# Performance work log

Measured on AMD Instinct MI355X. Metric: run time of the kernel, lower is better.

The kernel has to match this reference:

```python
import jax, jax.numpy as jnp
import numpy as np

B, M = 2, 8192          # clouds per batch, points per cloud (N = B*M)
K_NEAR, K_FAR, K_SMOOTH = 8, 16, 8
T_LOC, T_CON = 0.1, 0.5
EPS = 1e-8


def setup_inputs() -> dict:
    key = jax.random.key(0)
    k1, k2 = jax.random.split(key)
    scores = jax.random.uniform(k1, (B * M,), dtype=jnp.float32)          # in [0,1]
    coords = jax.random.normal(k2, (B * M, 3), dtype=jnp.float32) * 2.0   # point positions
    batch_ids = (jnp.arange(B * M, dtype=jnp.int32) // M).astype(jnp.int32)
    return {"scores": scores, "coords": coords, "batch_ids": batch_ids}


def _knn_global(coords):
    """Per-cloud brute-force kNN (self included as first neighbor, like pointops.knn_query).
    coords: (N,3) -> global indices (N, K_FAR)."""
    c = coords.reshape(B, M, 3)

    def per_cloud(cb):  # cb: (M,3)
        sq = jnp.sum(cb * cb, axis=-1)                      # (M,)
        d2 = sq[:, None] + sq[None, :] - 2.0 * (cb @ cb.T)  # (M,M) squared dists
        _, idx = jax.lax.top_k(-d2, K_FAR)                  # (M,K_FAR) smallest dists
        return idx

    idx = jax.vmap(per_cloud)(c)                            # (B,M,K_FAR) local indices
    idx = idx + (jnp.arange(B, dtype=idx.dtype) * M)[:, None, None]
    return idx.reshape(B * M, K_FAR)


def _loss_terms(scores, coords, idx):
    # --- locality: neighbors (incl. self) should have similar scores ---
    nb = idx[:, :K_NEAR]                                    # (N,k)
    score_diff = jnp.abs(scores[:, None] - scores[nb])      # (N,k)
    dists = jnp.linalg.norm(coords[:, None, :] - coords[nb], axis=2)  # (N,k)
    w = jnp.exp(-dists / T_LOC)
    loss_loc = jnp.sum(w * score_diff ** 2) / jnp.clip(jnp.sum(w), 1e-8)

    # --- contrastive: near similar, far dissimilar ---
    sim_pos = 1.0 - jnp.abs(scores[:, None] - scores[idx[:, :K_NEAR]])
    sim_neg = 1.0 - jnp.abs(scores[:, None] - scores[idx[:, K_NEAR:K_FAR]])
    loss_pos = -jnp.mean(jnp.log(jax.nn.sigmoid(sim_pos / T_CON) + EPS))
    loss_neg = -jnp.mean(jnp.log(1.0 - jax.nn.sigmoid(sim_neg / T_CON) + EPS))
    loss_con = loss_pos + loss_neg

    # --- distribution: sorted scores match uniform linspace per cloud ---
    sb = jnp.sort(scores.reshape(B, M), axis=1)             # (B,M)
    target = jnp.linspace(0.0, 1.0, M, dtype=scores.dtype)  # (M,)
    loss_dist = jnp.mean(jnp.mean((sb - target[None, :]) ** 2, axis=1))

    # --- smoothness: score close to neighbor mean ---
    nmean = jnp.mean(scores[idx[:, :K_SMOOTH]], axis=1)     # (N,)
    loss_smooth = jnp.mean((scores - nmean) ** 2)

    return loss_loc, loss_con, loss_dist, loss_smooth


def reference(scores, coords, batch_ids):
    del batch_ids  # equal-sized clouds; batch structure is (B, M) by construction
    idx = _knn_global(coords)
    l_loc, l_con, l_dist, l_smooth = _loss_terms(scores, coords, idx)
    total = 1.0 * l_loc + 0.5 * l_con + 0.3 * l_dist + 0.2 * l_smooth
    return total
```

## Files before the change

### kernel.cpp

```cpp
#include <hip/hip_runtime.h>
#include <math.h>

#define BB 2
#define MM 8192
#define NN (BB * MM)
#define NBATCH (NN / 16)
#define NCELL 4096
#define LOSS_BLOCKS 1024

#define PART_OFF   0
#define RANK_OFF   24576
#define IDX_OFF    90112
#define PK_OFF     1138688
#define SS_OFF     1400832
#define DONE_OFF   1466368
#define BBLO_OFF   1597440
#define BBHI_OFF   1613824

__device__ __forceinline__ unsigned mort3(unsigned x, unsigned y, unsigned z) {
    unsigned m = 0;
#pragma unroll
    for (int i = 0; i < 4; ++i) {
        m |= ((x >> i) & 1u) << (3 * i);
        m |= ((y >> i) & 1u) << (3 * i + 1);
        m |= ((z >> i) & 1u) << (3 * i + 2);
    }
    return m;
}

__global__ __launch_bounds__(1024) void prep_kernel(
    const float* __restrict__ coords, const float* __restrict__ scores,
    float4* __restrict__ pk_s, float* __restrict__ s_s,
    float4* __restrict__ bb_lo, float4* __restrict__ bb_hi,
    unsigned* __restrict__ done) {
    __shared__ int hist[NCELL];
    __shared__ int wsum[16];
    const int tid = threadIdx.x, blk = blockIdx.x;
    const int pbase = blk * MM;
    for (int i = tid; i < NCELL; i += 1024) hist[i] = 0;
    if (blk == 0 && tid == 0) *done = 0u;
    __syncthreads();

    int   cid[8];
    float px[8], py[8], pz[8];
#pragma unroll
    for (int it = 0; it < 8; ++it) {
        const int i = pbase + it * 1024 + tid;
        float x = coords[3 * i], y = coords[3 * i + 1], z = coords[3 * i + 2];
        int cx = min(15, max(0, (int)floorf(x) + 8));
        int cy = min(15, max(0, (int)floorf(y) + 8));
        int cz = min(15, max(0, (int)floorf(z) + 8));
        cid[it] = (int)mort3((unsigned)cx, (unsigned)cy, (unsigned)cz);
        px[it] = x; py[it] = y; pz[it] = z;
        atomicAdd(&hist[cid[it]], 1);
    }
    __syncthreads();

    int v[4]; int run = 0;
#pragma unroll
    for (int i = 0; i < 4; ++i) { int t = hist[tid * 4 + i]; v[i] = run; run += t; }
    const int lane = tid & 63, wv = tid >> 6;
    int inc = run;
#pragma unroll
    for (int off = 1; off < 64; off <<= 1) {
        int y = __shfl_up(inc, off);
        if (lane >= off) inc += y;
    }
    int laneExcl = inc - run;
    if (lane == 63) wsum[wv] = inc;
    __syncthreads();
    int wbase = 0;
#pragma unroll
    for (int w = 0; w < 16; ++w) wbase += (w < wv) ? wsum[w] : 0;
    const int base = wbase + laneExcl;
#pragma unroll
    for (int i = 0; i < 4; ++i) hist[tid * 4 + i] = base + v[i];
    __syncthreads();

#pragma unroll
    for (int it = 0; it < 8; ++it) {
        const int pos = pbase + atomicAdd(&hist[cid[it]], 1);
        const float x = px[it], y = py[it], z = pz[it];
        const float sq = fmaf(x, x, fmaf(y, y, z * z));
        pk_s[pos] = make_float4(x, y, z, sq);
        s_s[pos] = scores[pbase + it * 1024 + tid];
    }
    __syncthreads();

    if (tid < 512) {
        const int b = blk * 512 + tid;
        float4 c = pk_s[b * 16];
        float lx = c.x, ly = c.y, lz = c.z, hx = c.x, hy = c.y, hz = c.z;
#pragma unroll
        for (int i = 1; i < 16; ++i) {
            c = pk_s[b * 16 + i];
            lx = fminf(lx, c.x); ly = fminf(ly, c.y); lz = fminf(lz, c.z);
            hx = fmaxf(hx, c.x); hy = fmaxf(hy, c.y); hz = fmaxf(hz, c.z);
        }
        bb_lo[b] = make_float4(lx, ly, lz, 0.f);
        bb_hi[b] = make_float4(hx, hy, hz, 0.f);
    }
}

__device__ __forceinline__ void sort16(unsigned (&a)[16]) {
#pragma unroll
    for (int p2 = 1; p2 < 16; p2 <<= 1) {
#pragma unroll
        for (int k2 = p2; k2 >= 1; k2 >>= 1) {
#pragma unroll
            for (int j2 = k2 % p2; j2 + k2 < 16; j2 += 2 * k2) {
#pragma unroll
                for (int i2 = 0; i2 < k2; ++i2) {
                    if (i2 + j2 + k2 < 16) {
                        if (((i2 + j2) / (2 * p2)) == ((i2 + j2 + k2) / (2 * p2))) {
                            unsigned x = a[i2 + j2], y = a[i2 + j2 + k2];
                            a[i2 + j2]      = min(x, y);
                            a[i2 + j2 + k2] = max(x, y);
                        }
                    }
                }
            }
        }
    }
}

__device__ __forceinline__ void truncmerge(unsigned (&slot)[16], const unsigned (&kb)[16]) {
    unsigned m[16];
#pragma unroll
    for (int k = 0; k < 16; ++k) m[k] = min(slot[k], kb[15 - k]);
#pragma unroll
    for (int st = 8; st >= 1; st >>= 1) {
#pragma unroll
        for (int i = 0; i < 16; ++i) {
            if ((i & st) == 0) {
                unsigned lo = min(m[i], m[i + st]);
                unsigned hi = max(m[i], m[i + st]);
                m[i] = lo; m[i + st] = hi;
            }
        }
    }
#pragma unroll
    for (int k = 0; k < 16; ++k) slot[k] = m[k];
}

__global__ __launch_bounds__(1024) void knnrank_kernel(const float4* __restrict__ pk_s,
                                                       const float* __restrict__ s_s,
                                                       const float4* __restrict__ bb_lo,
                                                       const float4* __restrict__ bb_hi,
                                                       int* __restrict__ out_idx,
                                                       int* __restrict__ out_rank) {
    __shared__ unsigned lds_k[16][16][64];
    __shared__ int lds_aux[16][64];
    __shared__ unsigned lds_tmin[64];
    const int tid = threadIdx.x, lane = tid & 63;
    const int wv = __builtin_amdgcn_readfirstlane(tid >> 6);

    if (blockIdx.x >= 256) {
        const int qbase = (blockIdx.x - 256) << 6;
        const int cloudbase = (qbase >> 13) << 13;
        const float s = s_s[qbase + lane];
        const float* __restrict__ sc = s_s + cloudbase;
        int rk = 0;
        const int j0 = wv * 512;
        for (int jj = 0; jj < 512; jj += 16) {
#pragma unroll
            for (int i = 0; i < 16; ++i) {
                rk += (sc[j0 + jj + i] < s) ? 1 : 0;
            }
        }
        lds_aux[wv][lane] = rk;
        __syncthreads();
        if (wv == 0) {
            int rsum = 0;
#pragma unroll
            for (int w = 0; w < 16; ++w) rsum += lds_aux[w][lane];
            out_rank[qbase + lane] = rsum;
        }
        return;
    }

    const int qbase = blockIdx.x * 64;
    const int cloudbase = (qbase >> 13) << 13;
    const float4 p = pk_s[qbase + lane];
    const int sb0 = (qbase - cloudbase) >> 4;
    const float4* __restrict__ pc = pk_s + cloudbase;
    const int bbase = cloudbase >> 4;

    if (tid < 64) lds_tmin[tid] = 0x7f7fffffu;

    unsigned slot[16];
#pragma unroll
    for (int k = 0; k < 16; ++k) slot[k] = 0x7F000000u + (unsigned)k;
    float t_f = 3.0e38f;

    auto batch = [&](int bi) {
        unsigned kb[16];
#pragma unroll
        for (int i = 0; i < 16; ++i) {
            const int j = bi * 16 + i;
            const float4 c = pc[j];
            float dot = fmaf(p.x, c.x, fmaf(p.y, c.y, p.z * c.z));
            float d2  = fmaf(-2.0f, dot, p.w + c.w);
            kb[i] = (__float_as_uint(d2) & 0xFFFFE000u) | (unsigned)j;
        }
        sort16(kb);
        truncmerge(slot, kb);
        const unsigned nt = (slot[15] & 0xFFFFE000u) + 0x2000u;
        const float ntf = __uint_as_float(nt);
        if (ntf < t_f) {
            t_f = ntf;
            atomicMin(&lds_tmin[lane], nt);
        }
    };

    const int r = sb0 & 15;
    const int ownb = (wv >= r && wv < r + 4) ? (sb0 + (wv - r)) : -1;
    __syncthreads();
    if (ownb >= 0) batch(ownb);
    lds_aux[wv][lane] = (int)__float_as_uint(t_f);
    __syncthreads();
    float tb = __uint_as_float((unsigned)lds_aux[0][lane]);
#pragma unroll
    for (int w = 1; w < 16; ++w) tb = fminf(tb, __uint_as_float((unsigned)lds_aux[w][lane]));
    t_f = fminf(t_f, tb);

    float4 lo = bb_lo[bbase + wv];
    float4 hi = bb_hi[bbase + wv];
    for (int k = 0; k < 32; ++k) {
        const int bi = wv + (k << 4);
        float4 lo_n, hi_n;
        if (k + 1 < 32) {
            lo_n = bb_lo[bbase + bi + 16];
            hi_n = bb_hi[bbase + bi + 16];
        }
        if (bi != ownb) {
            const unsigned tmb = *((volatile unsigned*)&lds_tmin[lane]);
            const float tsh = fminf(t_f, __uint_as_float(tmb));
            float dx = fmaxf(fmaxf(lo.x - p.x, p.x - hi.x), 0.f);
            float dy = fmaxf(fmaxf(lo.y - p.y, p.y - hi.y), 0.f);
            float dz = fmaxf(fmaxf(lo.z - p.z, p.z - hi.z), 0.f);
            float lb = fmaf(dx, dx, fmaf(dy, dy, dz * dz));
            if (__any(fmaf(lb, 0.999f, -1e-5f) < tsh)) batch(bi);
        }
        lo = lo_n; hi = hi_n;
    }

#pragma unroll
    for (int k = 0; k < 16; ++k) lds_k[wv][k][lane] = slot[k];

    for (int half = 8; half >= 1; half >>= 1) {
        __syncthreads();
        if (wv < half) {
            unsigned a[16], m[16];
#pragma unroll
            for (int k = 0; k < 16; ++k) a[k] = lds_k[wv][k][lane];
#pragma unroll
            for (int k = 0; k < 16; ++k) m[k] = min(a[k], lds_k[wv + half][15 - k][lane]);
#pragma unroll
            for (int st = 8; st >= 1; st >>= 1) {
#pragma unroll
                for (int i = 0; i < 16; ++i) {
                    if ((i & st) == 0) {
                        unsigned lo2 = min(m[i], m[i + st]);
                        unsigned hi2 = max(m[i], m[i + st]);
                        m[i] = lo2; m[i + st] = hi2;
                    }
                }
            }
#pragma unroll
            for (int k = 0; k < 16; ++k) lds_k[wv][k][lane] = m[k];
        }
    }
    __syncthreads();

    if (wv == 0) {
#pragma unroll
        for (int k = 0; k < 16; ++k)
            out_idx[(qbase + lane) * 16 + k] = (int)(lds_k[0][k][lane] & 0x1FFFu) + cloudbase;
    }
}

__global__ __launch_bounds__(256) void lossfin_kernel(const float* __restrict__ s_s,
                                                      const float4* __restrict__ pk_s,
                                                      const int* __restrict__ knn,
                                                      const int* __restrict__ rnk,
                                                      float* __restrict__ partial,
                                                      unsigned* __restrict__ done,
                                                      float* __restrict__ out) {
    __shared__ float red[4][6];
    __shared__ float sgrp[16][6];
    __shared__ unsigned lastflag;
    const int t = blockIdx.x * 256 + threadIdx.x;
    const int q = t >> 4, k = t & 15;
    const int nb = knn[t];
    const float s  = s_s[q];
    const float sn = s_s[nb];
    const float diff = fabsf(s - sn);
    const float sim = 1.0f - diff;
    const float sg = 1.0f / (1.0f + expf(-2.0f * sim));

    float a_wd = 0.f, a_w = 0.f, a_pos = 0.f, a_neg = 0.f, snk = 0.f;
    if (k < 8) {
        float4 pq = pk_s[q];
        float4 pn = pk_s[nb];
        float dx = pq.x - pn.x, dy = pq.y - pn.y, dz = pq.z - pn.z;
        float d = sqrtf(dx * dx + dy * dy + dz * dz);
        float w = expf(-10.0f * d);
        a_wd = w * diff * diff;
        a_w  = w;
        a_pos = logf(sg + 1e-8f);
        snk = sn;
    } else {
        a_neg = logf(1.0f - sg + 1e-8f);
    }

    float nsum = snk;
#pragma unroll
    for (int off = 1; off < 16; off <<= 1) nsum += __shfl_xor(nsum, off);

    float a_sm = 0.f, a_di = 0.f;
    if (k == 0) {
        float t1 = s - nsum * 0.125f;
        a_sm = t1 * t1;
        float t2 = s - (float)rnk[q] * (1.0f / 8191.0f);
        a_di = t2 * t2;
    }

#pragma unroll
    for (int off = 1; off < 64; off <<= 1) {
        a_wd  += __shfl_xor(a_wd, off);
        a_w   += __shfl_xor(a_w, off);
        a_pos += __shfl_xor(a_pos, off);
        a_neg += __shfl_xor(a_neg, off);
        a_sm  += __shfl_xor(a_sm, off);
        a_di  += __shfl_xor(a_di, off);
    }
    const int wv = threadIdx.x >> 6;
    if ((threadIdx.x & 63) == 0) {
        red[wv][0] = a_wd; red[wv][1] = a_w; red[wv][2] = a_pos;
        red[wv][3] = a_neg; red[wv][4] = a_sm; red[wv][5] = a_di;
    }
    __syncthreads();
    if (threadIdx.x < 6) {
        float v = red[0][threadIdx.x] + red[1][threadIdx.x] +
                  red[2][threadIdx.x] + red[3][threadIdx.x];
        __hip_atomic_store(&partial[threadIdx.x * LOSS_BLOCKS + blockIdx.x], v,
                           __ATOMIC_RELEASE, __HIP_MEMORY_SCOPE_AGENT);
    }
    __syncthreads();
    if (threadIdx.x == 0)
        lastflag = __hip_atomic_fetch_add(done, 1u, __ATOMIC_ACQ_REL, __HIP_MEMORY_SCOPE_AGENT);
    __syncthreads();

    if (lastflag == (unsigned)(LOSS_BLOCKS - 1)) {
        const int tid = threadIdx.x, lane2 = tid & 63, w4 = tid >> 6;
#pragma unroll
        for (int rep = 0; rep < 4; ++rep) {
            const int w = w4 * 4 + rep;
            float a[6];
#pragma unroll
            for (int term = 0; term < 6; ++term)
                a[term] = __hip_atomic_load(&partial[term * LOSS_BLOCKS + w * 64 + lane2],
                                            __ATOMIC_ACQUIRE, __HIP_MEMORY_SCOPE_AGENT);
#pragma unroll
            for (int off = 1; off < 64; off <<= 1) {
#pragma unroll
                for (int term = 0; term < 6; ++term) a[term] += __shfl_xor(a[term], off);
            }
            if (lane2 == 0) {
#pragma unroll
                for (int term = 0; term < 6; ++term) sgrp[w][term] = a[term];
            }
        }
        __syncthreads();
        if (tid == 0) {
            float acc[6];
#pragma unroll
            for (int term = 0; term < 6; ++term) {
                float v = 0.f;
#pragma unroll
                for (int w = 0; w < 16; ++w) v += sgrp[w][term];
                acc[term] = v;
            }
            float l_loc = acc[0] / fmaxf(acc[1], 1e-8f);
            float l_pos = -acc[2] / (float)(NN * 8);
            float l_neg = -acc[3] / (float)(NN * 8);
            float l_sm  = acc[4] / (float)NN;
            float l_di  = acc[5] / (float)NN;
            out[0] = l_loc + 0.5f * (l_pos + l_neg) + 0.3f * l_di + 0.2f * l_sm;
        }
    }
}

extern "C" void kernel_launch(void* const* d_in, const int* in_sizes, int n_in,
                              void* d_out, int out_size, void* d_ws, size_t ws_size,
                              hipStream_t stream) {
    const float* scores = (const float*)d_in[0];
    const float* coords = (const float*)d_in[1];
    (void)in_sizes; (void)n_in; (void)out_size; (void)ws_size;

    char* ws = (char*)d_ws;
    float*  part  = (float*)(ws + PART_OFF);
    int*    rank  = (int*)(ws + RANK_OFF);
    int*    knn   = (int*)(ws + IDX_OFF);
    float4* pk_s  = (float4*)(ws + PK_OFF);
    float*  s_s   = (float*)(ws + SS_OFF);
    float4* bb_lo = (float4*)(ws + BBLO_OFF);
    float4* bb_hi = (float4*)(ws + BBHI_OFF);
    unsigned* done= (unsigned*)(ws + DONE_OFF);
    float*  out   = (float*)d_out;

    prep_kernel<<<2, 1024, 0, stream>>>(coords, scores, pk_s, s_s, bb_lo, bb_hi, done);
    knnrank_kernel<<<512, 1024, 0, stream>>>(pk_s, s_s, bb_lo, bb_hi, knn, rank);
    lossfin_kernel<<<LOSS_BLOCKS, 256, 0, stream>>>(s_s, pk_s, knn, rank, part, done, out);
}
```

Measured before the change: 168.1 us.

## Split prep kernel into histogram, global-atomic scatter, and bbox kernels

The single two-block prep kernel is split into three kernels. One computes cell ids and per-cell cursors, one scatters points into sorted order using global atomics across 64 blocks, and one computes per-16-point bounding boxes across 4 blocks. The aim is more parallelism than the two-block prep kernel had. The cost is two extra launches plus global round-trips for cell ids and cursors, and within-cell point order becomes nondeterministic.

```diff
diff --git a/kernel.cpp b/kernel.cpp
--- a/kernel.cpp
+++ b/kernel.cpp
@@ -13,9 +13,12 @@
 #define IDX_OFF    90112
 #define PK_OFF     1138688
 #define SS_OFF     1400832
-#define DONE_OFF   1466368
+#define CELLID_OFF 1466368
+#define CNT_OFF    1531904
+#define CUR_OFF    1564672
 #define BBLO_OFF   1597440
 #define BBHI_OFF   1613824
+#define DONE_OFF   1630208
 
 __device__ __forceinline__ unsigned mort3(unsigned x, unsigned y, unsigned z) {
     unsigned m = 0;
@@ -28,11 +31,9 @@
     return m;
 }
 
-__global__ __launch_bounds__(1024) void prep_kernel(
-    const float* __restrict__ coords, const float* __restrict__ scores,
-    float4* __restrict__ pk_s, float* __restrict__ s_s,
-    float4* __restrict__ bb_lo, float4* __restrict__ bb_hi,
-    unsigned* __restrict__ done) {
+__global__ __launch_bounds__(1024) void prepA_kernel(
+    const float* __restrict__ coords, int* __restrict__ cellid,
+    int* __restrict__ cursor, unsigned* __restrict__ done) {
     __shared__ int hist[NCELL];
     __shared__ int wsum[16];
     const int tid = threadIdx.x, blk = blockIdx.x;
@@ -41,8 +42,6 @@
     if (blk == 0 && tid == 0) *done = 0u;
     __syncthreads();
 
-    int   cid[8];
-    float px[8], py[8], pz[8];
 #pragma unroll
     for (int it = 0; it < 8; ++it) {
         const int i = pbase + it * 1024 + tid;
@@ -50,9 +49,9 @@
         int cx = min(15, max(0, (int)floorf(x) + 8));
         int cy = min(15, max(0, (int)floorf(y) + 8));
         int cz = min(15, max(0, (int)floorf(z) + 8));
-        cid[it] = (int)mort3((unsigned)cx, (unsigned)cy, (unsigned)cz);
-        px[it] = x; py[it] = y; pz[it] = z;
-        atomicAdd(&hist[cid[it]], 1);
+        const int c = (int)mort3((unsigned)cx, (unsigned)cy, (unsigned)cz);
+        cellid[i] = blk * NCELL + c;
+        atomicAdd(&hist[c], 1);
     }
     __syncthreads();
 
@@ -74,21 +73,27 @@
     for (int w = 0; w < 16; ++w) wbase += (w < wv) ? wsum[w] : 0;
     const int base = wbase + laneExcl;
 #pragma unroll
-    for (int i = 0; i < 4; ++i) hist[tid * 4 + i] = base + v[i];
-    __syncthreads();
-
-#pragma unroll
-    for (int it = 0; it < 8; ++it) {
-        const int pos = pbase + atomicAdd(&hist[cid[it]], 1);
-        const float x = px[it], y = py[it], z = pz[it];
-        const float sq = fmaf(x, x, fmaf(y, y, z * z));
+    for (int i = 0; i < 4; ++i)
+        cursor[blk * NCELL + tid * 4 + i] = pbase + base + v[i];
+}
+
+__global__ void scatter_kernel(const float* __restrict__ coords, const float* __restrict__ scores,
+                               const int* __restrict__ cellid, int* __restrict__ cursor,
+                               float4* __restrict__ pk_s, float* __restrict__ s_s) {
+    int i = blockIdx.x * 256 + threadIdx.x;
+    if (i < NN) {
+        int pos = atomicAdd(&cursor[cellid[i]], 1);
+        float x = coords[3 * i], y = coords[3 * i + 1], z = coords[3 * i + 2];
+        float sq = fmaf(x, x, fmaf(y, y, z * z));
         pk_s[pos] = make_float4(x, y, z, sq);
-        s_s[pos] = scores[pbase + it * 1024 + tid];
-    }
-    __syncthreads();
-
-    if (tid < 512) {
-        const int b = blk * 512 + tid;
+        s_s[pos] = scores[i];
+    }
+}
+
+__global__ void bbox_kernel(const float4* __restrict__ pk_s, float4* __restrict__ bb_lo,
+                            float4* __restrict__ bb_hi) {
+    int b = blockIdx.x * 256 + threadIdx.x;
+    if (b < NBATCH) {
         float4 c = pk_s[b * 16];
         float lx = c.x, ly = c.y, lz = c.z, hx = c.x, hy = c.y, hz = c.z;
 #pragma unroll
@@ -405,12 +410,16 @@
     int*    knn   = (int*)(ws + IDX_OFF);
     float4* pk_s  = (float4*)(ws + PK_OFF);
     float*  s_s   = (float*)(ws + SS_OFF);
+    int*    cellid= (int*)(ws + CELLID_OFF);
+    int*    cursor= (int*)(ws + CUR_OFF);
     float4* bb_lo = (float4*)(ws + BBLO_OFF);
     float4* bb_hi = (float4*)(ws + BBHI_OFF);
     unsigned* done= (unsigned*)(ws + DONE_OFF);
     float*  out   = (float*)d_out;
 
-    prep_kernel<<<2, 1024, 0, stream>>>(coords, scores, pk_s, s_s, bb_lo, bb_hi, done);
+    prepA_kernel<<<2, 1024, 0, stream>>>(coords, cellid, cursor, done);
+    scatter_kernel<<<64, 256, 0, stream>>>(coords, scores, cellid, cursor, pk_s, s_s);
+    bbox_kernel<<<4, 256, 0, stream>>>(pk_s, bb_lo, bb_hi);
     knnrank_kernel<<<512, 1024, 0, stream>>>(pk_s, s_s, bb_lo, bb_hi, knn, rank);
     lossfin_kernel<<<LOSS_BLOCKS, 256, 0, stream>>>(s_s, pk_s, knn, rank, part, done, out);
 }
```

Result: faster. 159.8 us (-4.9%).
